# Performance work log

Measured on AMD Instinct MI355X. Metric: run time of the kernel, lower is better.

The kernel has to match this reference:

```python
import jax, jax.numpy as jnp
import numpy as np
from jax import lax

NEG = -1e30  # log-domain 'zero'

B, T, D, V, L = 32, 800, 512, 1024, 100  # batch, frames, eprojs, odim, max label len


def setup_inputs() -> dict:
    key = jax.random.key(0)
    k0, k1, k2, k3, k4 = jax.random.split(key, 5)
    hpad = jax.random.normal(k0, (B, T, D), jnp.float32)
    W = jax.random.normal(k1, (V, D), jnp.float32) / np.sqrt(D).astype(np.float32)
    b = jnp.zeros((V,), jnp.float32)
    labels = jax.random.randint(k2, (B, L), 1, V, dtype=jnp.int32)  # blank=0 excluded
    ilens = jax.random.randint(k3, (B,), T // 2, T + 1, dtype=jnp.int32)
    label_lens = jax.random.randint(k4, (B,), L // 2, L + 1, dtype=jnp.int32)
    return {"hpad": hpad, "W": W, "b": b, "labels": labels,
            "ilens": ilens, "label_lens": label_lens}


def _ctc_loss(hpad, W, b, labels, ilens, label_lens):
    # ctc_lo: Linear(eprojs, odim); dropout_rate=0 -> identity
    logits = jnp.einsum('btd,vd->btv', hpad, W) + b          # [B,T,V]
    logp = jax.nn.log_softmax(logits, axis=-1)               # warp_ctc softmaxes acts internally
    Bb, Tt, Vv = logits.shape
    Ll = labels.shape[1]
    S = 2 * Ll + 1
    # extended label sequence with interleaved blanks (blank id = 0)
    ext = jnp.zeros((Bb, S), jnp.int32).at[:, 1::2].set(labels)  # [B,S]
    # gather log-probs of extended labels: [B,T,S] -> [T,B,S]
    lp_ext = jnp.take_along_axis(logp, jnp.broadcast_to(ext[:, None, :], (Bb, Tt, S)), axis=2)
    lp_seq = jnp.transpose(lp_ext, (1, 0, 2))                # [T,B,S]
    # skip transition s-2 -> s allowed iff ext[s] != blank and ext[s] != ext[s-2]
    ext_m2 = jnp.pad(ext, ((0, 0), (2, 0)))[:, :S]
    allow = (jnp.arange(S)[None, :] >= 2) & (ext != 0) & (ext != ext_m2)  # [B,S]

    # alpha init at t=0: positions 0 (blank) and 1 (first label)
    a0 = jnp.full((Bb, S), NEG, logp.dtype)
    a0 = a0.at[:, 0].set(lp_seq[0][:, 0])
    first = jnp.where(label_lens > 0, lp_seq[0][:, 1], NEG)
    a0 = a0.at[:, 1].set(first)

    def step(alpha, inp):
        lp_t, t = inp
        p1 = jnp.concatenate([jnp.full((Bb, 1), NEG, alpha.dtype), alpha[:, :-1]], axis=1)
        p2 = jnp.concatenate([jnp.full((Bb, 2), NEG, alpha.dtype), alpha[:, :-2]], axis=1)
        c = jnp.logaddexp(alpha, p1)
        c = jnp.where(allow, jnp.logaddexp(c, p2), c)
        new = c + lp_t
        active = (t < ilens)[:, None]  # frames past ilen leave alpha unchanged
        return jnp.where(active, new, alpha), None

    alphaT, _ = lax.scan(step, a0, (lp_seq[1:], jnp.arange(1, Tt)))

    idx_last = (2 * label_lens).astype(jnp.int32)            # ext index of final blank
    last = jnp.take_along_axis(alphaT, idx_last[:, None], axis=1)[:, 0]
    prev = jnp.take_along_axis(alphaT, jnp.maximum(idx_last - 1, 0)[:, None], axis=1)[:, 0]
    ll = jnp.logaddexp(last, jnp.where(label_lens > 0, prev, NEG))
    costs = -ll                                              # per-utterance NLL
    return jnp.sum(costs) / Bb                               # chainer-like: sum / batch


def reference(hpad, W, b, labels, ilens, label_lens):
    return _ctc_loss(hpad, W, b, labels, ilens, label_lens)
```

## Files before the change

### kernel.cpp

```cpp
#include <hip/hip_runtime.h>
#include <hip/hip_bf16.h>
#include <cstdint>

constexpr int CBATCH = 32;
constexpr int CT = 800;
constexpr int CD = 512;
constexpr int CV = 1024;
constexpr int CL = 100;
constexpr int CM = CBATCH * CT;
constexpr int CS = 2 * CL + 1;
constexpr int CSPL = 256;
constexpr float NEGV = -1e30f;
constexpr float INV_LN2 = 1.4426950408889634f;
constexpr float LN2F = 0.6931471805599453f;

typedef __bf16 bf16x8 __attribute__((ext_vector_type(8)));
typedef float f32x4 __attribute__((ext_vector_type(4)));
typedef unsigned short ushort8 __attribute__((ext_vector_type(8)));

__device__ inline unsigned short f2bf(float f) {
  union { float f; unsigned u; } v; v.f = f;
  unsigned u = v.u;
  unsigned r = (u + 0x7fffu + ((u >> 16) & 1u)) >> 16;
  return (unsigned short)r;
}
__device__ inline float bf2f(unsigned short u) {
  unsigned x = (unsigned)u << 16;
  return __builtin_bit_cast(float, x);
}

__device__ inline float fexp2(float x) { return __builtin_amdgcn_exp2f(x); }
__device__ inline float flog2(float x) { return __builtin_amdgcn_logf(x); }

__device__ inline float dpp_shr1(float x, float fill) {
  int r = __builtin_amdgcn_update_dpp(__builtin_bit_cast(int, fill),
                                      __builtin_bit_cast(int, x),
                                      0x138, 0xF, 0xF, false);
  return __builtin_bit_cast(float, r);
}
__device__ inline int dpp_shr1_int(int x, int fill) {
  return __builtin_amdgcn_update_dpp(fill, x, 0x138, 0xF, 0xF, false);
}
__device__ inline float dpp_shl1(float x, float fill) {
  int r = __builtin_amdgcn_update_dpp(__builtin_bit_cast(int, fill),
                                      __builtin_bit_cast(int, x),
                                      0x130, 0xF, 0xF, false);
  return __builtin_bit_cast(float, r);
}
__device__ inline int dpp_shl1_int(int x, int fill) {
  return __builtin_amdgcn_update_dpp(fill, x, 0x130, 0xF, 0xF, false);
}

__device__ inline void gload_lds16(const void* g, void* l) {
  __builtin_amdgcn_global_load_lds(
      (const __attribute__((address_space(1))) unsigned int*)g,
      (__attribute__((address_space(3))) unsigned int*)l, 16, 0, 0);
}

__global__ void cvt_kernel(const float* __restrict__ in, unsigned short* __restrict__ out, int n4) {
  int i = blockIdx.x * blockDim.x + threadIdx.x;
  if (i < n4) {
    float4 v = reinterpret_cast<const float4*>(in)[i];
    ushort4 o;
    o.x = f2bf(v.x); o.y = f2bf(v.y); o.z = f2bf(v.z); o.w = f2bf(v.w);
    reinterpret_cast<ushort4*>(out)[i] = o;
  }
}

constexpr int GBK = 64;

__global__ __launch_bounds__(256, 2) void gemm_kernel(
    const unsigned short* __restrict__ A,
    const unsigned short* __restrict__ Bt,
    const float* __restrict__ bias,
    unsigned short* __restrict__ C)
{
  __shared__ __align__(16) unsigned short As[128 * GBK];
  __shared__ __align__(16) unsigned short Bs[128 * GBK];
  const int tid = threadIdx.x;
  const int lane = tid & 63;
  const int wave = tid >> 6;
  const int wr = wave >> 1, wc = wave & 1;
  const int bm = blockIdx.x, bn = blockIdx.y;

  f32x4 acc[4][4] = {};

  for (int k0 = 0; k0 < CD; k0 += GBK) {
#pragma unroll
    for (int i = 0; i < 4; ++i) {
      int c = tid + 256 * i;
      int row = c >> 3;
      int scol = ((c & 7) ^ (row & 7)) * 8;
      gload_lds16(&A[(size_t)(bm * 128 + row) * CD + k0 + scol], &As[c * 8]);
      gload_lds16(&Bt[(size_t)(bn * 128 + row) * CD + k0 + scol], &Bs[c * 8]);
    }
    __syncthreads();
#pragma unroll
    for (int kk = 0; kk < 2; ++kk) {
      bf16x8 af[4], bfr[4];
#pragma unroll
      for (int m = 0; m < 4; ++m) {
        int row = wr * 64 + m * 16 + (lane & 15);
        int cb = kk * 4 + (lane >> 4);
        af[m] = *reinterpret_cast<const bf16x8*>(
            &As[row * GBK + (cb ^ (row & 7)) * 8]);
      }
#pragma unroll
      for (int n = 0; n < 4; ++n) {
        int row = wc * 64 + n * 16 + (lane & 15);
        int cb = kk * 4 + (lane >> 4);
        bfr[n] = *reinterpret_cast<const bf16x8*>(
            &Bs[row * GBK + (cb ^ (row & 7)) * 8]);
      }
#pragma unroll
      for (int m = 0; m < 4; ++m)
#pragma unroll
        for (int n = 0; n < 4; ++n)
          acc[m][n] = __builtin_amdgcn_mfma_f32_16x16x32_bf16(af[m], bfr[n], acc[m][n], 0, 0, 0);
    }
    __syncthreads();
  }

  float bv[4];
#pragma unroll
  for (int n = 0; n < 4; ++n)
    bv[n] = bias[bn * 128 + wc * 64 + n * 16 + (lane & 15)];
#pragma unroll
  for (int m = 0; m < 4; ++m) {
    int rbase = bm * 128 + wr * 64 + m * 16 + (lane >> 4) * 4;
#pragma unroll
    for (int n = 0; n < 4; ++n) {
      int col = bn * 128 + wc * 64 + n * 16 + (lane & 15);
#pragma unroll
      for (int r = 0; r < 4; ++r)
        C[(size_t)(rbase + r) * CV + col] = f2bf(acc[m][n][r] + bv[n]);
    }
  }
}

__global__ void lse_gather_kernel(const unsigned short* __restrict__ C,
                                  const int* __restrict__ labels,
                                  float* __restrict__ lpg) {
  const int wave = threadIdx.x >> 6, lane = threadIdx.x & 63;
  const int row = blockIdx.x * 4 + wave;
  const int b = row / CT;
  const unsigned short* p = C + (size_t)row * CV;
  ushort8 v0 = reinterpret_cast<const ushort8*>(p)[lane * 2];
  ushort8 v1 = reinterpret_cast<const ushort8*>(p)[lane * 2 + 1];
  float f[16];
#pragma unroll
  for (int i = 0; i < 8; ++i) { f[i] = bf2f(v0[i]); f[8 + i] = bf2f(v1[i]); }
  float m = f[0];
#pragma unroll
  for (int i = 1; i < 16; ++i) m = fmaxf(m, f[i]);
#pragma unroll
  for (int off = 32; off >= 1; off >>= 1) m = fmaxf(m, __shfl_xor(m, off));
  float s = 0.f;
#pragma unroll
  for (int i = 0; i < 16; ++i) s += __expf(f[i] - m);
#pragma unroll
  for (int off = 32; off >= 1; off >>= 1) s += __shfl_xor(s, off);
  const float l = m + __logf(s);

  float4 o;
  if (lane < 51) {
    const int* lab = labels + b * CL;
    const int s0 = lane * 4;
    float vals[4];
#pragma unroll
    for (int j = 0; j < 4; ++j) {
      int st = s0 + j;
      if (st >= CS) { vals[j] = NEGV; continue; }
      int e = (st & 1) ? lab[st >> 1] : 0;
      vals[j] = (bf2f(p[e]) - l) * INV_LN2;
    }
    o.x = fexp2(vals[0]); o.y = fexp2(vals[1]);
    o.z = fexp2(vals[2]); o.w = fexp2(vals[3]);
  } else {
    o.x = o.y = o.z = o.w = 0.f;
  }
  reinterpret_cast<float4*>(lpg + (size_t)row * CSPL)[lane] = o;
}

constexpr int RRING = 64;
constexpr int NCHUNKS = 51;

__global__ __launch_bounds__(256, 1) void ctc_kernel(
    const float* __restrict__ lpg, const int* __restrict__ labels,
    const int* __restrict__ ilens, const int* __restrict__ llens,
    float* __restrict__ abuf, int* __restrict__ kbuf) {
  __shared__ __align__(16) float ring[RRING * CSPL];
  __shared__ int ready[NCHUNKS + 1];
  __shared__ int done;
  const int bq = blockIdx.x;
  const int b = bq >> 1, dir = bq & 1;
  const int tid = threadIdx.x;
  const int lane = tid & 63;
  const int wid = tid >> 6;
  const float* base = lpg + (size_t)b * CT * CSPL;

  for (int i = tid; i < NCHUNKS + 1; i += 256) ready[i] = 0;
  if (tid == 0) done = 0;
  __syncthreads();

  if (wid == 0) {
    const int ilen = ilens[b];
    const int ll = llens[b];
    const int* lab = labels + b * CL;
    const int s0 = lane * 4;
    float m1f = 0.f, m3f = 0.f;
    if (lane < 51) {
      int s1 = s0 + 1;
      if (s1 >= 3 && s1 < CS && lab[s1 >> 1] != lab[(s1 >> 1) - 1]) m1f = 1.f;
      int s3 = s0 + 3;
      if (s3 < CS && lab[s3 >> 1] != lab[(s3 >> 1) - 1]) m3f = 1.f;
    }
    float a0, a1, a2, a3;
    int kk = 0;
    if (dir == 0) {
      f32x4 r0 = reinterpret_cast<const f32x4*>(base)[lane];
      a0 = (lane == 0) ? r0[0] : 0.f;
      a1 = (lane == 0 && ll > 0) ? r0[1] : 0.f;
      a2 = 0.f; a3 = 0.f;
    } else {
      const int e1 = 2 * ll, e2 = 2 * ll - 1;
      a0 = (s0 + 0 == e1 || s0 + 0 == e2) ? 1.f : 0.f;
      a1 = (s0 + 1 == e1 || s0 + 1 == e2) ? 1.f : 0.f;
      a2 = (s0 + 2 == e1 || s0 + 2 == e2) ? 1.f : 0.f;
      a3 = (s0 + 3 == e1 || s0 + 3 == e2) ? 1.f : 0.f;
    }

    volatile int* rdy = ready;
    while (rdy[0] == 0) {}
    asm volatile("" ::: "memory");
    f32x4 lpA = *reinterpret_cast<const f32x4*>(&ring[0 * CSPL + lane * 4]);
    f32x4 lpB = *reinterpret_cast<const f32x4*>(&ring[1 * CSPL + lane * 4]);
    f32x4 lpC = *reinterpret_cast<const f32x4*>(&ring[2 * CSPL + lane * 4]);
    f32x4 lpD = *reinterpret_cast<const f32x4*>(&ring[3 * CSPL + lane * 4]);
    f32x4 lpE = *reinterpret_cast<const f32x4*>(&ring[4 * CSPL + lane * 4]);
    f32x4 lpF = *reinterpret_cast<const f32x4*>(&ring[5 * CSPL + lane * 4]);
    f32x4 lpG = *reinterpret_cast<const f32x4*>(&ring[6 * CSPL + lane * 4]);
    f32x4 lpH = *reinterpret_cast<const f32x4*>(&ring[7 * CSPL + lane * 4]);

#define FSTEP(LP, J)                                                      \
    {                                                                     \
      const int u_ = uc + (J);                                            \
      f32x4 cur_ = LP;                                                    \
      LP = *reinterpret_cast<const f32x4*>(                               \
          &ring[((u_ + 8) & (RRING - 1)) * CSPL + lane * 4]);             \
      float nm_ = dpp_shr1(a3, 0.f);                                      \
      int nk_ = dpp_shr1_int(kk, (int)0xE0000000);                        \
      if (1 + u_ < ilen) {                                                \
        int K_ = nk_ > kk ? nk_ : kk;                                     \
        int ta_ = kk - K_ + 127;                                          \
        int tn_ = nk_ - K_ + 127;                                         \
        float fa_ = ta_ > 0 ? __builtin_bit_cast(float, ta_ << 23) : 0.f; \
        float fn_ = tn_ > 0 ? __builtin_bit_cast(float, tn_ << 23) : 0.f; \
        float na3_ = nm_ * fn_;                                           \
        float c0_ = __builtin_fmaf(a0, fa_, na3_);                        \
        float c1_ = __builtin_fmaf(a0 + a1, fa_, na3_ * m1f);             \
        float c2_ = (a1 + a2) * fa_;                                      \
        float c3_ = __builtin_fmaf(a1, m3f, a2 + a3) * fa_;               \
        a0 = c0_ * cur_[0]; a1 = c1_ * cur_[1];                           \
        a2 = c2_ * cur_[2]; a3 = c3_ * cur_[3];                           \
        float mm_ = fmaxf(fmaxf(a0, a1), fmaxf(a2, a3));                  \
        int e_ = (__builtin_bit_cast(int, mm_) >> 23) & 0xFF;             \
        float sc_ = __builtin_bit_cast(float, (254 - e_) << 23);          \
        a0 *= sc_; a1 *= sc_; a2 *= sc_; a3 *= sc_;                       \
        kk = K_ + e_ - 127;                                               \
      }                                                                   \
    }

#define BSTEP(LP, J)                                                      \
    {                                                                     \
      const int u_ = uc + (J);                                            \
      const int r_ = 799 - u_;                                            \
      f32x4 q_ = LP;                                                      \
      LP = *reinterpret_cast<const f32x4*>(                               \
          &ring[((u_ + 8) & (RRING - 1)) * CSPL + lane * 4]);             \
      float g0_ = a0 * q_[0], g1_ = a1 * q_[1];                           \
      float g2_ = a2 * q_[2], g3_ = a3 * q_[3];                           \
      float h_ = __builtin_fmaf(g1_, m1f, g0_);                           \
      float hn_ = dpp_shl1(h_, 0.f);                                      \
      int nk_ = dpp_shl1_int(kk, (int)0xE0000000);                        \
      if (r_ > 400 && r_ < ilen) {                                        \
        int K_ = nk_ > kk ? nk_ : kk;                                     \
        int ta_ = kk - K_ + 127;                                          \
        int tn_ = nk_ - K_ + 127;                                         \
        float fa_ = ta_ > 0 ? __builtin_bit_cast(float, ta_ << 23) : 0.f; \
        float fn_ = tn_ > 0 ? __builtin_bit_cast(float, tn_ << 23) : 0.f; \
        float c0_ = (g0_ + g1_) * fa_;                                    \
        float c1_ = __builtin_fmaf(g3_, m3f, g1_ + g2_) * fa_;            \
        float c2_ = (g2_ + g3_) * fa_;                                    \
        float c3_ = __builtin_fmaf(hn_, fn_, g3_ * fa_);                  \
        a0 = c0_; a1 = c1_; a2 = c2_; a3 = c3_;                           \
        float mm_ = fmaxf(fmaxf(a0, a1), fmaxf(a2, a3));                  \
        int e_ = (__builtin_bit_cast(int, mm_) >> 23) & 0xFF;             \
        float sc_ = __builtin_bit_cast(float, (254 - e_) << 23);          \
        a0 *= sc_; a1 *= sc_; a2 *= sc_; a3 *= sc_;                       \
        kk = K_ + e_ - 127;                                               \
      }                                                                   \
    }

    if (dir == 0) {
      for (int c = 0; c < 50; ++c) {
        while (rdy[c] == 0) {}
        while (rdy[c + 1] == 0) {}
        asm volatile("" ::: "memory");
        const int uc = 8 * c;
        FSTEP(lpA, 0) FSTEP(lpB, 1) FSTEP(lpC, 2) FSTEP(lpD, 3)
        FSTEP(lpE, 4) FSTEP(lpF, 5) FSTEP(lpG, 6) FSTEP(lpH, 7)
        asm volatile("s_waitcnt lgkmcnt(0)" ::: "memory");
        if (lane == 0) *(volatile int*)&done = c + 1;
      }
    } else {
      for (int c = 0; c < 50; ++c) {
        while (rdy[c] == 0) {}
        while (rdy[c + 1] == 0) {}
        asm volatile("" ::: "memory");
        const int uc = 8 * c;
        BSTEP(lpA, 0) BSTEP(lpB, 1) BSTEP(lpC, 2) BSTEP(lpD, 3)
        BSTEP(lpE, 4) BSTEP(lpF, 5) BSTEP(lpG, 6) BSTEP(lpH, 7)
        asm volatile("s_waitcnt lgkmcnt(0)" ::: "memory");
        if (lane == 0) *(volatile int*)&done = c + 1;
      }
    }
#undef FSTEP
#undef BSTEP

    const int idx = bq * 64 + lane;
    f32x4 mv; mv[0] = a0; mv[1] = a1; mv[2] = a2; mv[3] = a3;
    reinterpret_cast<f32x4*>(abuf)[idx] = mv;
    kbuf[idx] = kk;
  } else {
    const int p = wid - 1;
    for (int c = p; c < NCHUNKS; c += 3) {
      if (c >= 8) {
        while (*(volatile int*)&done < c - 7) {}
      }
      asm volatile("" ::: "memory");
      const int i0 = 8 * c;
      const float* src = base + (size_t)(dir ? (799 - i0) : (1 + i0)) * CSPL;
      const ptrdiff_t strd = dir ? -(ptrdiff_t)CSPL : (ptrdiff_t)CSPL;
      f32x4 v0 = reinterpret_cast<const f32x4*>(src + 0 * strd)[lane];
      f32x4 v1 = reinterpret_cast<const f32x4*>(src + 1 * strd)[lane];
      f32x4 v2 = reinterpret_cast<const f32x4*>(src + 2 * strd)[lane];
      f32x4 v3 = reinterpret_cast<const f32x4*>(src + 3 * strd)[lane];
      f32x4 v4 = reinterpret_cast<const f32x4*>(src + 4 * strd)[lane];
      f32x4 v5 = reinterpret_cast<const f32x4*>(src + 5 * strd)[lane];
      f32x4 v6 = reinterpret_cast<const f32x4*>(src + 6 * strd)[lane];
      f32x4 v7 = reinterpret_cast<const f32x4*>(src + 7 * strd)[lane];
      float* dst = &ring[((i0) & (RRING - 1)) * CSPL + lane * 4];
      *reinterpret_cast<f32x4*>(dst + 0 * CSPL) = v0;
      *reinterpret_cast<f32x4*>(dst + 1 * CSPL) = v1;
      *reinterpret_cast<f32x4*>(dst + 2 * CSPL) = v2;
      *reinterpret_cast<f32x4*>(dst + 3 * CSPL) = v3;
      *reinterpret_cast<f32x4*>(dst + 4 * CSPL) = v4;
      *reinterpret_cast<f32x4*>(dst + 5 * CSPL) = v5;
      *reinterpret_cast<f32x4*>(dst + 6 * CSPL) = v6;
      *reinterpret_cast<f32x4*>(dst + 7 * CSPL) = v7;
      asm volatile("s_waitcnt lgkmcnt(0)" ::: "memory");
      if (lane == 0) *(volatile int*)&ready[c] = 1;
    }
  }
}

__global__ void combine_kernel(const float* __restrict__ abuf,
                               const int* __restrict__ kbuf,
                               float* __restrict__ out) {
  const int b = blockIdx.x;
  const int lane = threadIdx.x;
  f32x4 am = reinterpret_cast<const f32x4*>(abuf)[(b * 2 + 0) * 64 + lane];
  f32x4 bm = reinterpret_cast<const f32x4*>(abuf)[(b * 2 + 1) * 64 + lane];
  int ak = kbuf[(b * 2 + 0) * 64 + lane];
  int bk = kbuf[(b * 2 + 1) * 64 + lane];
  float val = am[0] * bm[0] + am[1] * bm[1] + am[2] * bm[2] + am[3] * bm[3];
  int e = (val > 0.f) ? (ak + bk) : (int)0xC0000000;
  int E = e;
#pragma unroll
  for (int off = 32; off >= 1; off >>= 1) E = max(E, __shfl_xor(E, off));
  int t = e - E + 127;
  float f = t > 0 ? __builtin_bit_cast(float, t << 23) : 0.f;
  float c = val * f;
#pragma unroll
  for (int off = 32; off >= 1; off >>= 1) c += __shfl_xor(c, off);
  if (lane == 0) {
    float ll2 = flog2(c) + (float)E;
    atomicAdd(out, -ll2 * (LN2F / CBATCH));
  }
}

extern "C" void kernel_launch(void* const* d_in, const int* in_sizes, int n_in,
                              void* d_out, int out_size, void* d_ws, size_t ws_size,
                              hipStream_t stream) {
  const float* hpad = (const float*)d_in[0];
  const float* W    = (const float*)d_in[1];
  const float* bias = (const float*)d_in[2];
  const int* labels = (const int*)d_in[3];
  const int* ilens  = (const int*)d_in[4];
  const int* llens  = (const int*)d_in[5];
  float* out = (float*)d_out;

  char* ws = (char*)d_ws;
  size_t off = 0;
  auto alloc = [&](size_t bytes) -> void* {
    void* p = ws + off;
    off = (off + bytes + 255) & ~(size_t)255;
    return p;
  };
  unsigned short* Abf = (unsigned short*)alloc((size_t)CM * CD * 2);
  unsigned short* Wbf = (unsigned short*)alloc((size_t)CV * CD * 2);
  unsigned short* logits = (unsigned short*)alloc((size_t)CM * CV * 2);
  float* lpg  = (float*)alloc((size_t)(CM + 64) * CSPL * 4);
  float* abuf = (float*)alloc((size_t)CBATCH * 2 * 64 * 4 * sizeof(float));
  int*   kbuf = (int*)alloc((size_t)CBATCH * 2 * 64 * sizeof(int));

  hipMemsetAsync(d_out, 0, sizeof(float), stream);

  cvt_kernel<<<(CM * CD / 4 + 255) / 256, 256, 0, stream>>>(hpad, Abf, CM * CD / 4);
  cvt_kernel<<<(CV * CD / 4 + 255) / 256, 256, 0, stream>>>(W, Wbf, CV * CD / 4);
  gemm_kernel<<<dim3(CM / 128, CV / 128), 256, 0, stream>>>(Abf, Wbf, bias, logits);
  lse_gather_kernel<<<CM / 4, 256, 0, stream>>>(logits, labels, lpg);
  ctc_kernel<<<CBATCH * 2, 256, 0, stream>>>(lpg, labels, ilens, llens, abuf, kbuf);
  combine_kernel<<<CBATCH, 64, 0, stream>>>(abuf, kbuf, out);
}
```

Baseline: 117.3 us.

## Fuse two CTC recursion time steps into one composed update per iteration

Rewrites the forward and backward alpha/beta recursions so each iteration applies two time steps at once. The two-step transition is expanded algebraically, with neighbour lane values fetched by DPP shifts, so one renormalisation and one cross-lane exchange cover two frames. This shortens the serial dependency chain on the latency-bound single wave. The cost is more multiplies per step, extra DPP moves, and fallback branches for frames near ilen and the midpoint boundary.

```diff
diff --git a/kernel.cpp b/kernel.cpp
--- a/kernel.cpp
+++ b/kernel.cpp
@@ -28,6 +28,7 @@
   unsigned x = (unsigned)u << 16;
   return __builtin_bit_cast(float, x);
 }
+__device__ inline float bitf(int x) { return __builtin_bit_cast(float, x); }
 
 __device__ inline float fexp2(float x) { return __builtin_amdgcn_exp2f(x); }
 __device__ inline float flog2(float x) { return __builtin_amdgcn_logf(x); }
@@ -215,6 +216,12 @@
       int s3 = s0 + 3;
       if (s3 < CS && lab[s3 >> 1] != lab[(s3 >> 1) - 1]) m3f = 1.f;
     }
+    const float Mm1 = dpp_shr1(m3f, 0.f);
+    const float M1Mm1 = m1f * Mm1;
+    const float M3M1 = m3f * m1f;
+    const float nM1 = dpp_shl1(m1f, 0.f);
+    const float nM3 = dpp_shl1(m3f, 0.f);
+
     float a0, a1, a2, a3;
     int kk = 0;
     if (dir == 0) {
@@ -242,64 +249,123 @@
     f32x4 lpG = *reinterpret_cast<const f32x4*>(&ring[6 * CSPL + lane * 4]);
     f32x4 lpH = *reinterpret_cast<const f32x4*>(&ring[7 * CSPL + lane * 4]);
 
-#define FSTEP(LP, J)                                                      \
-    {                                                                     \
-      const int u_ = uc + (J);                                            \
-      f32x4 cur_ = LP;                                                    \
-      LP = *reinterpret_cast<const f32x4*>(                               \
-          &ring[((u_ + 8) & (RRING - 1)) * CSPL + lane * 4]);             \
-      float nm_ = dpp_shr1(a3, 0.f);                                      \
-      int nk_ = dpp_shr1_int(kk, (int)0xE0000000);                        \
-      if (1 + u_ < ilen) {                                                \
-        int K_ = nk_ > kk ? nk_ : kk;                                     \
-        int ta_ = kk - K_ + 127;                                          \
-        int tn_ = nk_ - K_ + 127;                                         \
-        float fa_ = ta_ > 0 ? __builtin_bit_cast(float, ta_ << 23) : 0.f; \
-        float fn_ = tn_ > 0 ? __builtin_bit_cast(float, tn_ << 23) : 0.f; \
-        float na3_ = nm_ * fn_;                                           \
-        float c0_ = __builtin_fmaf(a0, fa_, na3_);                        \
-        float c1_ = __builtin_fmaf(a0 + a1, fa_, na3_ * m1f);             \
-        float c2_ = (a1 + a2) * fa_;                                      \
-        float c3_ = __builtin_fmaf(a1, m3f, a2 + a3) * fa_;               \
-        a0 = c0_ * cur_[0]; a1 = c1_ * cur_[1];                           \
-        a2 = c2_ * cur_[2]; a3 = c3_ * cur_[3];                           \
-        float mm_ = fmaxf(fmaxf(a0, a1), fmaxf(a2, a3));                  \
-        int e_ = (__builtin_bit_cast(int, mm_) >> 23) & 0xFF;             \
-        float sc_ = __builtin_bit_cast(float, (254 - e_) << 23);          \
-        a0 *= sc_; a1 *= sc_; a2 *= sc_; a3 *= sc_;                       \
-        kk = K_ + e_ - 127;                                               \
-      }                                                                   \
-    }
-
-#define BSTEP(LP, J)                                                      \
-    {                                                                     \
-      const int u_ = uc + (J);                                            \
-      const int r_ = 799 - u_;                                            \
-      f32x4 q_ = LP;                                                      \
-      LP = *reinterpret_cast<const f32x4*>(                               \
-          &ring[((u_ + 8) & (RRING - 1)) * CSPL + lane * 4]);             \
-      float g0_ = a0 * q_[0], g1_ = a1 * q_[1];                           \
-      float g2_ = a2 * q_[2], g3_ = a3 * q_[3];                           \
-      float h_ = __builtin_fmaf(g1_, m1f, g0_);                           \
-      float hn_ = dpp_shl1(h_, 0.f);                                      \
-      int nk_ = dpp_shl1_int(kk, (int)0xE0000000);                        \
-      if (r_ > 400 && r_ < ilen) {                                        \
-        int K_ = nk_ > kk ? nk_ : kk;                                     \
-        int ta_ = kk - K_ + 127;                                          \
-        int tn_ = nk_ - K_ + 127;                                         \
-        float fa_ = ta_ > 0 ? __builtin_bit_cast(float, ta_ << 23) : 0.f; \
-        float fn_ = tn_ > 0 ? __builtin_bit_cast(float, tn_ << 23) : 0.f; \
-        float c0_ = (g0_ + g1_) * fa_;                                    \
-        float c1_ = __builtin_fmaf(g3_, m3f, g1_ + g2_) * fa_;            \
-        float c2_ = (g2_ + g3_) * fa_;                                    \
-        float c3_ = __builtin_fmaf(hn_, fn_, g3_ * fa_);                  \
-        a0 = c0_; a1 = c1_; a2 = c2_; a3 = c3_;                           \
-        float mm_ = fmaxf(fmaxf(a0, a1), fmaxf(a2, a3));                  \
-        int e_ = (__builtin_bit_cast(int, mm_) >> 23) & 0xFF;             \
-        float sc_ = __builtin_bit_cast(float, (254 - e_) << 23);          \
-        a0 *= sc_; a1 *= sc_; a2 *= sc_; a3 *= sc_;                       \
-        kk = K_ + e_ - 127;                                               \
-      }                                                                   \
+#define RENORM2                                                            \
+      {                                                                    \
+        float mm_ = fmaxf(fmaxf(a0, a1), fmaxf(a2, a3));                   \
+        int e_ = (__builtin_bit_cast(int, mm_) >> 23) & 0xFF;              \
+        float sc_ = bitf((254 - e_) << 23);                                \
+        a0 *= sc_; a1 *= sc_; a2 *= sc_; a3 *= sc_;                        \
+        kk = K_ + e_ - 127;                                                \
+      }
+
+#define ALIGNF                                                             \
+      int K_ = nk_ > kk ? nk_ : kk;                                        \
+      int ta_ = kk - K_ + 127, tn_ = nk_ - K_ + 127;                       \
+      float fa_ = ta_ > 0 ? bitf(ta_ << 23) : 0.f;                         \
+      float fn_ = tn_ > 0 ? bitf(tn_ << 23) : 0.f;
+
+#define FITER(L1, L2, I)                                                   \
+    {                                                                      \
+      const int u1_ = 2 * (I);                                             \
+      f32x4 q1_ = L1, q2_ = L2;                                            \
+      L1 = *reinterpret_cast<const f32x4*>(                                \
+          &ring[((u1_ + 8) & 63) * CSPL + lane * 4]);                      \
+      L2 = *reinterpret_cast<const f32x4*>(                                \
+          &ring[((u1_ + 9) & 63) * CSPL + lane * 4]);                      \
+      float pa1_ = dpp_shr1(a1, 0.f);                                      \
+      float pa2_ = dpp_shr1(a2, 0.f);                                      \
+      float pa3_ = dpp_shr1(a3, 0.f);                                      \
+      int nk_ = dpp_shr1_int(kk, (int)0xE0000000);                         \
+      float Pm1_ = dpp_shr1(q1_[3], 0.f);                                  \
+      if (2 + u1_ < ilen) {                                                \
+        ALIGNF                                                             \
+        float A0_ = a0 * fa_, A1_ = a1 * fa_;                              \
+        float A2_ = a2 * fa_, A3_ = a3 * fa_;                              \
+        float N1_ = pa1_ * fn_, N2_ = pa2_ * fn_, N3_ = pa3_ * fn_;        \
+        float P0_ = q1_[0], P1_ = q1_[1], P2_ = q1_[2], P3_ = q1_[3];      \
+        float v0_ = P0_ * A0_ + (P0_ + Pm1_) * N3_ + Pm1_ * N2_            \
+                  + (Mm1 * Pm1_) * N1_;                                    \
+        float v1_ = P1_ * A1_ + (P1_ + P0_) * A0_                          \
+                  + __builtin_fmaf(m1f, P1_ + Pm1_, P0_) * N3_             \
+                  + (m1f * Pm1_) * N2_ + (M1Mm1 * Pm1_) * N1_;             \
+        float v2_ = P2_ * A2_ + (P2_ + P1_) * A1_ + P1_ * A0_              \
+                  + (m1f * P1_) * N3_;                                     \
+        float v3_ = P3_ * A3_ + (P3_ + P2_) * A2_                          \
+                  + __builtin_fmaf(m3f, P3_ + P1_, P2_) * A1_              \
+                  + (m3f * P1_) * A0_ + (M3M1 * P1_) * N3_;                \
+        a0 = v0_ * q2_[0]; a1 = v1_ * q2_[1];                              \
+        a2 = v2_ * q2_[2]; a3 = v3_ * q2_[3];                              \
+        RENORM2                                                            \
+      } else {                  \
+        ALIGNF                                                             \
+        float na3_ = pa3_ * fn_;                                           \
+        float c0_ = __builtin_fmaf(a0, fa_, na3_);                         \
+        float c1_ = __builtin_fmaf(a0 + a1, fa_, na3_ * m1f);              \
+        float c2_ = (a1 + a2) * fa_;                                       \
+        float c3_ = __builtin_fmaf(a1, m3f, a2 + a3) * fa_;                \
+        a0 = c0_ * q1_[0]; a1 = c1_ * q1_[1];                              \
+        a2 = c2_ * q1_[2]; a3 = c3_ * q1_[3];                              \
+        RENORM2                                                            \
+      }                                                                    \
+    }
+
+#define BS1(Q, QN0, QN1)                                                   \
+      {                                                                    \
+        ALIGNF                                                             \
+        float g0_ = a0 * Q[0], g1_ = a1 * Q[1];                            \
+        float g2_ = a2 * Q[2], g3_ = a3 * Q[3];                            \
+        float hn_ = QN0 * nb0_ + (nM1 * QN1) * nb1_;                       \
+        a0 = (g0_ + g1_) * fa_;                                            \
+        a1 = __builtin_fmaf(g3_, m3f, g1_ + g2_) * fa_;                    \
+        a2 = (g2_ + g3_) * fa_;                                            \
+        a3 = __builtin_fmaf(hn_, fn_, g3_ * fa_);                          \
+        RENORM2                                                            \
+      }
+
+#define BITER(L1, L2, I)                                                   \
+    {                                                                      \
+      const int u1_ = 2 * (I);                                             \
+      const int r1_ = 799 - u1_, r2_ = 798 - u1_;                          \
+      f32x4 q1_ = L1, q2_ = L2;                                            \
+      L1 = *reinterpret_cast<const f32x4*>(                                \
+          &ring[((u1_ + 8) & 63) * CSPL + lane * 4]);                      \
+      L2 = *reinterpret_cast<const f32x4*>(                                \
+          &ring[((u1_ + 9) & 63) * CSPL + lane * 4]);                      \
+      float nb0_ = dpp_shl1(a0, 0.f), nb1_ = dpp_shl1(a1, 0.f);            \
+      float nb2_ = dpp_shl1(a2, 0.f), nb3_ = dpp_shl1(a3, 0.f);            \
+      int nk_ = dpp_shl1_int(kk, (int)0xE0000000);                         \
+      float Q1n0_ = dpp_shl1(q1_[0], 0.f), Q1n1_ = dpp_shl1(q1_[1], 0.f);  \
+      float Q1n2_ = dpp_shl1(q1_[2], 0.f), Q1n3_ = dpp_shl1(q1_[3], 0.f);  \
+      float Q2n0_ = dpp_shl1(q2_[0], 0.f), Q2n1_ = dpp_shl1(q2_[1], 0.f);  \
+      const bool g1g_ = (r1_ < ilen);                 \
+      const bool g2g_ = (r2_ > 400) && (r2_ < ilen);                       \
+      if (g1g_ && g2g_) {                                                  \
+        ALIGNF                                                             \
+        float B0_ = a0 * fa_, B1_ = a1 * fa_;                              \
+        float B2_ = a2 * fa_, B3_ = a3 * fa_;                              \
+        float N0_ = nb0_ * fn_, N1_ = nb1_ * fn_;                          \
+        float N2_ = nb2_ * fn_, N3_ = nb3_ * fn_;                          \
+        float Q10_ = q1_[0], Q11_ = q1_[1], Q12_ = q1_[2], Q13_ = q1_[3];  \
+        float Q20_ = q2_[0], Q21_ = q2_[1], Q22_ = q2_[2], Q23_ = q2_[3];  \
+        float w0_ = (Q20_ * Q10_) * B0_ + ((Q20_ + Q21_) * Q11_) * B1_     \
+                  + (Q21_ * Q12_) * B2_ + (m3f * Q21_ * Q13_) * B3_;       \
+        float w1_ = (Q21_ * Q11_) * B1_ + ((Q21_ + Q22_) * Q12_) * B2_     \
+                  + (__builtin_fmaf(m3f, Q21_ + Q23_, Q22_) * Q13_) * B3_  \
+                  + (m3f * Q23_ * Q1n0_) * N0_                             \
+                  + (m3f * nM1 * Q23_ * Q1n1_) * N1_;                      \
+        float w2_ = (Q22_ * Q12_) * B2_ + ((Q22_ + Q23_) * Q13_) * B3_     \
+                  + (Q23_ * Q1n0_) * N0_ + (nM1 * Q23_ * Q1n1_) * N1_;     \
+        float w3_ = (Q23_ * Q13_) * B3_ + ((Q23_ + Q2n0_) * Q1n0_) * N0_   \
+                  + (__builtin_fmaf(nM1, Q23_ + Q2n1_, Q2n0_) * Q1n1_) * N1_ \
+                  + (nM1 * Q2n1_ * Q1n2_) * N2_                            \
+                  + (nM1 * nM3 * Q2n1_ * Q1n3_) * N3_;                     \
+        a0 = w0_; a1 = w1_; a2 = w2_; a3 = w3_;                            \
+        RENORM2                                                            \
+      } else if (g1g_) {                                                   \
+        BS1(q1_, Q1n0_, Q1n1_)                                             \
+      } else if (g2g_) {                                                   \
+        BS1(q2_, Q2n0_, Q2n1_)                                             \
+      }                                                                    \
     }
 
     if (dir == 0) {
@@ -307,9 +373,11 @@
         while (rdy[c] == 0) {}
         while (rdy[c + 1] == 0) {}
         asm volatile("" ::: "memory");
-        const int uc = 8 * c;
-        FSTEP(lpA, 0) FSTEP(lpB, 1) FSTEP(lpC, 2) FSTEP(lpD, 3)
-        FSTEP(lpE, 4) FSTEP(lpF, 5) FSTEP(lpG, 6) FSTEP(lpH, 7)
+        const int i0 = 4 * c;
+        FITER(lpA, lpB, i0 + 0)
+        FITER(lpC, lpD, i0 + 1)
+        FITER(lpE, lpF, i0 + 2)
+        FITER(lpG, lpH, i0 + 3)
         asm volatile("s_waitcnt lgkmcnt(0)" ::: "memory");
         if (lane == 0) *(volatile int*)&done = c + 1;
       }
@@ -318,15 +386,20 @@
         while (rdy[c] == 0) {}
         while (rdy[c + 1] == 0) {}
         asm volatile("" ::: "memory");
-        const int uc = 8 * c;
-        BSTEP(lpA, 0) BSTEP(lpB, 1) BSTEP(lpC, 2) BSTEP(lpD, 3)
-        BSTEP(lpE, 4) BSTEP(lpF, 5) BSTEP(lpG, 6) BSTEP(lpH, 7)
+        const int i0 = 4 * c;
+        BITER(lpA, lpB, i0 + 0)
+        BITER(lpC, lpD, i0 + 1)
+        BITER(lpE, lpF, i0 + 2)
+        BITER(lpG, lpH, i0 + 3)
         asm volatile("s_waitcnt lgkmcnt(0)" ::: "memory");
         if (lane == 0) *(volatile int*)&done = c + 1;
       }
     }
-#undef FSTEP
-#undef BSTEP
+#undef FITER
+#undef BITER
+#undef BS1
+#undef ALIGNF
+#undef RENORM2
 
     const int idx = bq * 64 + lane;
     f32x4 mv; mv[0] = a0; mv[1] = a1; mv[2] = a2; mv[3] = a3;
```

After: 133.0 us. 13.4% more time.

## Interleave forward and backward CTC recursions in one wavefront per utterance

Applied to the files above, without the earlier changes.

The CTC kernel used two blocks per utterance, one for the forward and one for the backward half. It now uses a single block per utterance: one wavefront runs both recursions with their steps interleaved, so the two independent dependency chains can hide each other's latency. Loader wavefronts fill two half-size LDS rings, one per direction, and the prefetch distance is reduced to fit. This halves the grid to 32 blocks and doubles register pressure in the compute wave, and the loaders now have less lead time over the consumer.

```diff
diff --git a/kernel.cpp b/kernel.cpp
--- a/kernel.cpp
+++ b/kernel.cpp
@@ -28,6 +28,7 @@
   unsigned x = (unsigned)u << 16;
   return __builtin_bit_cast(float, x);
 }
+__device__ inline float bitf(int x) { return __builtin_bit_cast(float, x); }
 
 __device__ inline float fexp2(float x) { return __builtin_amdgcn_exp2f(x); }
 __device__ inline float flog2(float x) { return __builtin_amdgcn_logf(x); }
@@ -182,18 +183,18 @@
   reinterpret_cast<float4*>(lpg + (size_t)row * CSPL)[lane] = o;
 }
 
-constexpr int RRING = 64;
+constexpr int HRING = 32;
 constexpr int NCHUNKS = 51;
 
 __global__ __launch_bounds__(256, 1) void ctc_kernel(
     const float* __restrict__ lpg, const int* __restrict__ labels,
     const int* __restrict__ ilens, const int* __restrict__ llens,
     float* __restrict__ abuf, int* __restrict__ kbuf) {
-  __shared__ __align__(16) float ring[RRING * CSPL];
+  __shared__ __align__(16) float ringF[HRING * CSPL];
+  __shared__ __align__(16) float ringB[HRING * CSPL];
   __shared__ int ready[NCHUNKS + 1];
   __shared__ int done;
-  const int bq = blockIdx.x;
-  const int b = bq >> 1, dir = bq & 1;
+  const int b = blockIdx.x;
   const int tid = threadIdx.x;
   const int lane = tid & 63;
   const int wid = tid >> 6;
@@ -215,59 +216,65 @@
       int s3 = s0 + 3;
       if (s3 < CS && lab[s3 >> 1] != lab[(s3 >> 1) - 1]) m3f = 1.f;
     }
-    float a0, a1, a2, a3;
-    int kk = 0;
-    if (dir == 0) {
-      f32x4 r0 = reinterpret_cast<const f32x4*>(base)[lane];
-      a0 = (lane == 0) ? r0[0] : 0.f;
-      a1 = (lane == 0 && ll > 0) ? r0[1] : 0.f;
-      a2 = 0.f; a3 = 0.f;
-    } else {
-      const int e1 = 2 * ll, e2 = 2 * ll - 1;
-      a0 = (s0 + 0 == e1 || s0 + 0 == e2) ? 1.f : 0.f;
-      a1 = (s0 + 1 == e1 || s0 + 1 == e2) ? 1.f : 0.f;
-      a2 = (s0 + 2 == e1 || s0 + 2 == e2) ? 1.f : 0.f;
-      a3 = (s0 + 3 == e1 || s0 + 3 == e2) ? 1.f : 0.f;
-    }
+
+    f32x4 r0 = reinterpret_cast<const f32x4*>(base)[lane];
+    float fa0 = (lane == 0) ? r0[0] : 0.f;
+    float fa1 = (lane == 0 && ll > 0) ? r0[1] : 0.f;
+    float fa2 = 0.f, fa3 = 0.f;
+    int fkk = 0;
+    const int e1 = 2 * ll, e2 = 2 * ll - 1;
+    float ba0 = (s0 + 0 == e1 || s0 + 0 == e2) ? 1.f : 0.f;
+    float ba1 = (s0 + 1 == e1 || s0 + 1 == e2) ? 1.f : 0.f;
+    float ba2 = (s0 + 2 == e1 || s0 + 2 == e2) ? 1.f : 0.f;
+    float ba3 = (s0 + 3 == e1 || s0 + 3 == e2) ? 1.f : 0.f;
+    int bkk = 0;
 
     volatile int* rdy = ready;
     while (rdy[0] == 0) {}
     asm volatile("" ::: "memory");
-    f32x4 lpA = *reinterpret_cast<const f32x4*>(&ring[0 * CSPL + lane * 4]);
-    f32x4 lpB = *reinterpret_cast<const f32x4*>(&ring[1 * CSPL + lane * 4]);
-    f32x4 lpC = *reinterpret_cast<const f32x4*>(&ring[2 * CSPL + lane * 4]);
-    f32x4 lpD = *reinterpret_cast<const f32x4*>(&ring[3 * CSPL + lane * 4]);
-    f32x4 lpE = *reinterpret_cast<const f32x4*>(&ring[4 * CSPL + lane * 4]);
-    f32x4 lpF = *reinterpret_cast<const f32x4*>(&ring[5 * CSPL + lane * 4]);
-    f32x4 lpG = *reinterpret_cast<const f32x4*>(&ring[6 * CSPL + lane * 4]);
-    f32x4 lpH = *reinterpret_cast<const f32x4*>(&ring[7 * CSPL + lane * 4]);
+    f32x4 fA = *reinterpret_cast<const f32x4*>(&ringF[0 * CSPL + lane * 4]);
+    f32x4 fB = *reinterpret_cast<const f32x4*>(&ringF[1 * CSPL + lane * 4]);
+    f32x4 fC = *reinterpret_cast<const f32x4*>(&ringF[2 * CSPL + lane * 4]);
+    f32x4 fD = *reinterpret_cast<const f32x4*>(&ringF[3 * CSPL + lane * 4]);
+    f32x4 fE = *reinterpret_cast<const f32x4*>(&ringF[4 * CSPL + lane * 4]);
+    f32x4 fF = *reinterpret_cast<const f32x4*>(&ringF[5 * CSPL + lane * 4]);
+    f32x4 fG = *reinterpret_cast<const f32x4*>(&ringF[6 * CSPL + lane * 4]);
+    f32x4 fH = *reinterpret_cast<const f32x4*>(&ringF[7 * CSPL + lane * 4]);
+    f32x4 bA = *reinterpret_cast<const f32x4*>(&ringB[0 * CSPL + lane * 4]);
+    f32x4 bB = *reinterpret_cast<const f32x4*>(&ringB[1 * CSPL + lane * 4]);
+    f32x4 bC = *reinterpret_cast<const f32x4*>(&ringB[2 * CSPL + lane * 4]);
+    f32x4 bD = *reinterpret_cast<const f32x4*>(&ringB[3 * CSPL + lane * 4]);
+    f32x4 bE = *reinterpret_cast<const f32x4*>(&ringB[4 * CSPL + lane * 4]);
+    f32x4 bF = *reinterpret_cast<const f32x4*>(&ringB[5 * CSPL + lane * 4]);
+    f32x4 bG = *reinterpret_cast<const f32x4*>(&ringB[6 * CSPL + lane * 4]);
+    f32x4 bH = *reinterpret_cast<const f32x4*>(&ringB[7 * CSPL + lane * 4]);
 
 #define FSTEP(LP, J)                                                      \
     {                                                                     \
       const int u_ = uc + (J);                                            \
       f32x4 cur_ = LP;                                                    \
       LP = *reinterpret_cast<const f32x4*>(                               \
-          &ring[((u_ + 8) & (RRING - 1)) * CSPL + lane * 4]);             \
-      float nm_ = dpp_shr1(a3, 0.f);                                      \
-      int nk_ = dpp_shr1_int(kk, (int)0xE0000000);                        \
+          &ringF[((u_ + 8) & (HRING - 1)) * CSPL + lane * 4]);            \
+      float nm_ = dpp_shr1(fa3, 0.f);                                     \
+      int nk_ = dpp_shr1_int(fkk, (int)0xE0000000);                       \
       if (1 + u_ < ilen) {                                                \
-        int K_ = nk_ > kk ? nk_ : kk;                                     \
-        int ta_ = kk - K_ + 127;                                          \
+        int K_ = nk_ > fkk ? nk_ : fkk;                                   \
+        int ta_ = fkk - K_ + 127;                                         \
         int tn_ = nk_ - K_ + 127;                                         \
-        float fa_ = ta_ > 0 ? __builtin_bit_cast(float, ta_ << 23) : 0.f; \
-        float fn_ = tn_ > 0 ? __builtin_bit_cast(float, tn_ << 23) : 0.f; \
+        float fa_ = ta_ > 0 ? bitf(ta_ << 23) : 0.f;                      \
+        float fn_ = tn_ > 0 ? bitf(tn_ << 23) : 0.f;                      \
         float na3_ = nm_ * fn_;                                           \
-        float c0_ = __builtin_fmaf(a0, fa_, na3_);                        \
-        float c1_ = __builtin_fmaf(a0 + a1, fa_, na3_ * m1f);             \
-        float c2_ = (a1 + a2) * fa_;                                      \
-        float c3_ = __builtin_fmaf(a1, m3f, a2 + a3) * fa_;               \
-        a0 = c0_ * cur_[0]; a1 = c1_ * cur_[1];                           \
-        a2 = c2_ * cur_[2]; a3 = c3_ * cur_[3];                           \
-        float mm_ = fmaxf(fmaxf(a0, a1), fmaxf(a2, a3));                  \
+        float c0_ = __builtin_fmaf(fa0, fa_, na3_);                       \
+        float c1_ = __builtin_fmaf(fa0 + fa1, fa_, na3_ * m1f);           \
+        float c2_ = (fa1 + fa2) * fa_;                                    \
+        float c3_ = __builtin_fmaf(fa1, m3f, fa2 + fa3) * fa_;            \
+        fa0 = c0_ * cur_[0]; fa1 = c1_ * cur_[1];                         \
+        fa2 = c2_ * cur_[2]; fa3 = c3_ * cur_[3];                         \
+        float mm_ = fmaxf(fmaxf(fa0, fa1), fmaxf(fa2, fa3));              \
         int e_ = (__builtin_bit_cast(int, mm_) >> 23) & 0xFF;             \
-        float sc_ = __builtin_bit_cast(float, (254 - e_) << 23);          \
-        a0 *= sc_; a1 *= sc_; a2 *= sc_; a3 *= sc_;                       \
-        kk = K_ + e_ - 127;                                               \
+        float sc_ = bitf((254 - e_) << 23);                               \
+        fa0 *= sc_; fa1 *= sc_; fa2 *= sc_; fa3 *= sc_;                   \
+        fkk = K_ + e_ - 127;                                              \
       }                                                                   \
     }
 
@@ -277,88 +284,96 @@
       const int r_ = 799 - u_;                                            \
       f32x4 q_ = LP;                                                      \
       LP = *reinterpret_cast<const f32x4*>(                               \
-          &ring[((u_ + 8) & (RRING - 1)) * CSPL + lane * 4]);             \
-      float g0_ = a0 * q_[0], g1_ = a1 * q_[1];                           \
-      float g2_ = a2 * q_[2], g3_ = a3 * q_[3];                           \
+          &ringB[((u_ + 8) & (HRING - 1)) * CSPL + lane * 4]);            \
+      float g0_ = ba0 * q_[0], g1_ = ba1 * q_[1];                         \
+      float g2_ = ba2 * q_[2], g3_ = ba3 * q_[3];                         \
       float h_ = __builtin_fmaf(g1_, m1f, g0_);                           \
       float hn_ = dpp_shl1(h_, 0.f);                                      \
-      int nk_ = dpp_shl1_int(kk, (int)0xE0000000);                        \
+      int nk_ = dpp_shl1_int(bkk, (int)0xE0000000);                       \
       if (r_ > 400 && r_ < ilen) {                                        \
-        int K_ = nk_ > kk ? nk_ : kk;                                     \
-        int ta_ = kk - K_ + 127;                                          \
+        int K_ = nk_ > bkk ? nk_ : bkk;                                   \
+        int ta_ = bkk - K_ + 127;                                         \
         int tn_ = nk_ - K_ + 127;                                         \
-        float fa_ = ta_ > 0 ? __builtin_bit_cast(float, ta_ << 23) : 0.f; \
-        float fn_ = tn_ > 0 ? __builtin_bit_cast(float, tn_ << 23) : 0.f; \
+        float fa_ = ta_ > 0 ? bitf(ta_ << 23) : 0.f;                      \
+        float fn_ = tn_ > 0 ? bitf(tn_ << 23) : 0.f;                      \
         float c0_ = (g0_ + g1_) * fa_;                                    \
         float c1_ = __builtin_fmaf(g3_, m3f, g1_ + g2_) * fa_;            \
         float c2_ = (g2_ + g3_) * fa_;                                    \
         float c3_ = __builtin_fmaf(hn_, fn_, g3_ * fa_);                  \
-        a0 = c0_; a1 = c1_; a2 = c2_; a3 = c3_;                           \
-        float mm_ = fmaxf(fmaxf(a0, a1), fmaxf(a2, a3));                  \
+        ba0 = c0_; ba1 = c1_; ba2 = c2_; ba3 = c3_;                       \
+        float mm_ = fmaxf(fmaxf(ba0, ba1), fmaxf(ba2, ba3));              \
         int e_ = (__builtin_bit_cast(int, mm_) >> 23) & 0xFF;             \
-        float sc_ = __builtin_bit_cast(float, (254 - e_) << 23);          \
-        a0 *= sc_; a1 *= sc_; a2 *= sc_; a3 *= sc_;                       \
-        kk = K_ + e_ - 127;                                               \
+        float sc_ = bitf((254 - e_) << 23);                               \
+        ba0 *= sc_; ba1 *= sc_; ba2 *= sc_; ba3 *= sc_;                   \
+        bkk = K_ + e_ - 127;                                              \
       }                                                                   \
     }
 
-    if (dir == 0) {
-      for (int c = 0; c < 50; ++c) {
-        while (rdy[c] == 0) {}
-        while (rdy[c + 1] == 0) {}
-        asm volatile("" ::: "memory");
-        const int uc = 8 * c;
-        FSTEP(lpA, 0) FSTEP(lpB, 1) FSTEP(lpC, 2) FSTEP(lpD, 3)
-        FSTEP(lpE, 4) FSTEP(lpF, 5) FSTEP(lpG, 6) FSTEP(lpH, 7)
-        asm volatile("s_waitcnt lgkmcnt(0)" ::: "memory");
-        if (lane == 0) *(volatile int*)&done = c + 1;
-      }
-    } else {
-      for (int c = 0; c < 50; ++c) {
-        while (rdy[c] == 0) {}
-        while (rdy[c + 1] == 0) {}
-        asm volatile("" ::: "memory");
-        const int uc = 8 * c;
-        BSTEP(lpA, 0) BSTEP(lpB, 1) BSTEP(lpC, 2) BSTEP(lpD, 3)
-        BSTEP(lpE, 4) BSTEP(lpF, 5) BSTEP(lpG, 6) BSTEP(lpH, 7)
-        asm volatile("s_waitcnt lgkmcnt(0)" ::: "memory");
-        if (lane == 0) *(volatile int*)&done = c + 1;
-      }
+    for (int c = 0; c < 50; ++c) {
+      while (rdy[c] == 0) {}
+      while (rdy[c + 1] == 0) {}
+      asm volatile("" ::: "memory");
+      const int uc = 8 * c;
+      FSTEP(fA, 0) BSTEP(bA, 0) FSTEP(fB, 1) BSTEP(bB, 1)
+      FSTEP(fC, 2) BSTEP(bC, 2) FSTEP(fD, 3) BSTEP(bD, 3)
+      FSTEP(fE, 4) BSTEP(bE, 4) FSTEP(fF, 5) BSTEP(bF, 5)
+      FSTEP(fG, 6) BSTEP(bG, 6) FSTEP(fH, 7) BSTEP(bH, 7)
+      asm volatile("s_waitcnt lgkmcnt(0)" ::: "memory");
+      if (lane == 0) *(volatile int*)&done = c + 1;
     }
 #undef FSTEP
 #undef BSTEP
 
-    const int idx = bq * 64 + lane;
-    f32x4 mv; mv[0] = a0; mv[1] = a1; mv[2] = a2; mv[3] = a3;
-    reinterpret_cast<f32x4*>(abuf)[idx] = mv;
-    kbuf[idx] = kk;
+    f32x4 mf; mf[0] = fa0; mf[1] = fa1; mf[2] = fa2; mf[3] = fa3;
+    f32x4 mb; mb[0] = ba0; mb[1] = ba1; mb[2] = ba2; mb[3] = ba3;
+    reinterpret_cast<f32x4*>(abuf)[(b * 2 + 0) * 64 + lane] = mf;
+    reinterpret_cast<f32x4*>(abuf)[(b * 2 + 1) * 64 + lane] = mb;
+    kbuf[(b * 2 + 0) * 64 + lane] = fkk;
+    kbuf[(b * 2 + 1) * 64 + lane] = bkk;
   } else {
     const int p = wid - 1;
     for (int c = p; c < NCHUNKS; c += 3) {
-      if (c >= 8) {
-        while (*(volatile int*)&done < c - 7) {}
+      if (c >= 4) {
+        while (*(volatile int*)&done < c - 3) {}
       }
       asm volatile("" ::: "memory");
       const int i0 = 8 * c;
-      const float* src = base + (size_t)(dir ? (799 - i0) : (1 + i0)) * CSPL;
-      const ptrdiff_t strd = dir ? -(ptrdiff_t)CSPL : (ptrdiff_t)CSPL;
-      f32x4 v0 = reinterpret_cast<const f32x4*>(src + 0 * strd)[lane];
-      f32x4 v1 = reinterpret_cast<const f32x4*>(src + 1 * strd)[lane];
-      f32x4 v2 = reinterpret_cast<const f32x4*>(src + 2 * strd)[lane];
-      f32x4 v3 = reinterpret_cast<const f32x4*>(src + 3 * strd)[lane];
-      f32x4 v4 = reinterpret_cast<const f32x4*>(src + 4 * strd)[lane];
-      f32x4 v5 = reinterpret_cast<const f32x4*>(src + 5 * strd)[lane];
-      f32x4 v6 = reinterpret_cast<const f32x4*>(src + 6 * strd)[lane];
-      f32x4 v7 = reinterpret_cast<const f32x4*>(src + 7 * strd)[lane];
-      float* dst = &ring[((i0) & (RRING - 1)) * CSPL + lane * 4];
-      *reinterpret_cast<f32x4*>(dst + 0 * CSPL) = v0;
-      *reinterpret_cast<f32x4*>(dst + 1 * CSPL) = v1;
-      *reinterpret_cast<f32x4*>(dst + 2 * CSPL) = v2;
-      *reinterpret_cast<f32x4*>(dst + 3 * CSPL) = v3;
-      *reinterpret_cast<f32x4*>(dst + 4 * CSPL) = v4;
-      *reinterpret_cast<f32x4*>(dst + 5 * CSPL) = v5;
-      *reinterpret_cast<f32x4*>(dst + 6 * CSPL) = v6;
-      *reinterpret_cast<f32x4*>(dst + 7 * CSPL) = v7;
+      const float* fsrc = base + (size_t)(1 + i0) * CSPL;
+      const float* bsrc = base + (size_t)(799 - i0) * CSPL;
+      f32x4 w0 = reinterpret_cast<const f32x4*>(fsrc + 0 * CSPL)[lane];
+      f32x4 w1 = reinterpret_cast<const f32x4*>(fsrc + 1 * CSPL)[lane];
+      f32x4 w2 = reinterpret_cast<const f32x4*>(fsrc + 2 * CSPL)[lane];
+      f32x4 w3 = reinterpret_cast<const f32x4*>(fsrc + 3 * CSPL)[lane];
+      f32x4 w4 = reinterpret_cast<const f32x4*>(fsrc + 4 * CSPL)[lane];
+      f32x4 w5 = reinterpret_cast<const f32x4*>(fsrc + 5 * CSPL)[lane];
+      f32x4 w6 = reinterpret_cast<const f32x4*>(fsrc + 6 * CSPL)[lane];
+      f32x4 w7 = reinterpret_cast<const f32x4*>(fsrc + 7 * CSPL)[lane];
+      f32x4 x0 = reinterpret_cast<const f32x4*>(bsrc - 0 * CSPL)[lane];
+      f32x4 x1 = reinterpret_cast<const f32x4*>(bsrc - 1 * CSPL)[lane];
+      f32x4 x2 = reinterpret_cast<const f32x4*>(bsrc - 2 * CSPL)[lane];
+      f32x4 x3 = reinterpret_cast<const f32x4*>(bsrc - 3 * CSPL)[lane];
+      f32x4 x4 = reinterpret_cast<const f32x4*>(bsrc - 4 * CSPL)[lane];
+      f32x4 x5 = reinterpret_cast<const f32x4*>(bsrc - 5 * CSPL)[lane];
+      f32x4 x6 = reinterpret_cast<const f32x4*>(bsrc - 6 * CSPL)[lane];
+      f32x4 x7 = reinterpret_cast<const f32x4*>(bsrc - 7 * CSPL)[lane];
+      float* fdst = &ringF[(i0 & (HRING - 1)) * CSPL + lane * 4];
+      float* bdst = &ringB[(i0 & (HRING - 1)) * CSPL + lane * 4];
+      *reinterpret_cast<f32x4*>(fdst + 0 * CSPL) = w0;
+      *reinterpret_cast<f32x4*>(fdst + 1 * CSPL) = w1;
+      *reinterpret_cast<f32x4*>(fdst + 2 * CSPL) = w2;
+      *reinterpret_cast<f32x4*>(fdst + 3 * CSPL) = w3;
+      *reinterpret_cast<f32x4*>(fdst + 4 * CSPL) = w4;
+      *reinterpret_cast<f32x4*>(fdst + 5 * CSPL) = w5;
+      *reinterpret_cast<f32x4*>(fdst + 6 * CSPL) = w6;
+      *reinterpret_cast<f32x4*>(fdst + 7 * CSPL) = w7;
+      *reinterpret_cast<f32x4*>(bdst + 0 * CSPL) = x0;
+      *reinterpret_cast<f32x4*>(bdst + 1 * CSPL) = x1;
+      *reinterpret_cast<f32x4*>(bdst + 2 * CSPL) = x2;
+      *reinterpret_cast<f32x4*>(bdst + 3 * CSPL) = x3;
+      *reinterpret_cast<f32x4*>(bdst + 4 * CSPL) = x4;
+      *reinterpret_cast<f32x4*>(bdst + 5 * CSPL) = x5;
+      *reinterpret_cast<f32x4*>(bdst + 6 * CSPL) = x6;
+      *reinterpret_cast<f32x4*>(bdst + 7 * CSPL) = x7;
       asm volatile("s_waitcnt lgkmcnt(0)" ::: "memory");
       if (lane == 0) *(volatile int*)&ready[c] = 1;
     }
@@ -421,6 +436,6 @@
   cvt_kernel<<<(CV * CD / 4 + 255) / 256, 256, 0, stream>>>(W, Wbf, CV * CD / 4);
   gemm_kernel<<<dim3(CM / 128, CV / 128), 256, 0, stream>>>(Abf, Wbf, bias, logits);
   lse_gather_kernel<<<CM / 4, 256, 0, stream>>>(logits, labels, lpg);
-  ctc_kernel<<<CBATCH * 2, 256, 0, stream>>>(lpg, labels, ilens, llens, abuf, kbuf);
+  ctc_kernel<<<CBATCH, 256, 0, stream>>>(lpg, labels, ilens, llens, abuf, kbuf);
   combine_kernel<<<CBATCH, 64, 0, stream>>>(abuf, kbuf, out);
 }
```

Measured after the change: 144.5 us. 23.2% more time.
